# Optimization experiments

Measured on AMD Instinct MI355X. Metric: run time of the kernel, lower is better.

The kernel has to match this reference:

```python
import jax, jax.numpy as jnp
import numpy as np

N = 50000   # nodes
E = 800000  # directed edges (self-loops added inside reference)
F_IN, H, C = 128, 96, 32


def setup_inputs() -> dict:
    key = jax.random.key(0)
    ks = jax.random.split(key, 8)
    x = jax.random.normal(ks[0], (N, F_IN), dtype=jnp.float32)
    edge_index = jax.random.randint(ks[1], (2, E), 0, N, dtype=jnp.int64)
    W1 = jax.random.normal(ks[2], (F_IN, H), dtype=jnp.float32) * 0.05
    b1 = jnp.zeros((H,), dtype=jnp.float32)
    W2 = jax.random.normal(ks[3], (H, H), dtype=jnp.float32) * 0.05
    b2 = jnp.zeros((H,), dtype=jnp.float32)
    W3 = jax.random.normal(ks[4], (H, C), dtype=jnp.float32) * 0.05
    b3 = jnp.zeros((C,), dtype=jnp.float32)
    return {"x": x, "edge_index": edge_index, "W1": W1, "b1": b1,
            "W2": W2, "b2": b2, "W3": W3, "b3": b3}


def gcn_conv(x, W, b, src, dst, n):
    """PyG GCNConv: x' = D^{-1/2} (A+I) D^{-1/2} (x W) + b (self-loops in src/dst)."""
    xw = x @ W                                        # [n, out]
    ones = jnp.ones(src.shape[0], dtype=xw.dtype)
    deg = jax.ops.segment_sum(ones, dst, num_segments=n)
    dinv = jnp.where(deg > 0, jax.lax.rsqrt(jnp.maximum(deg, 1.0)), 0.0)
    norm = dinv[src] * dinv[dst]                      # [E+n]
    msg = norm[:, None] * xw[src]                     # gather + scale
    out = jax.ops.segment_sum(msg, dst, num_segments=n)  # scatter-add
    return out + b


def reference(x, edge_index, W1, b1, W2, b2, W3, b3):
    loop = jnp.arange(N, dtype=edge_index.dtype)
    src = jnp.concatenate([edge_index[0], loop])      # add self-loops once
    dst = jnp.concatenate([edge_index[1], loop])
    h = jax.nn.relu(gcn_conv(x, W1, b1, src, dst, N))   # dropout is identity (eval)
    h = jax.nn.relu(gcn_conv(h, W2, b2, src, dst, N))
    h = gcn_conv(h, W3, b3, src, dst, N)
    return jax.nn.log_softmax(h, axis=1)
```

## Files before the change

### kernel.cpp

```cpp
#include <hip/hip_runtime.h>
#include <hip/hip_fp16.h>


typedef _Float16 half8 __attribute__((ext_vector_type(8)));
typedef float f32x4 __attribute__((ext_vector_type(4)));

constexpr int CAP = 64;
constexpr int NPB = 128;
constexpr int NBINS_P = 512;
constexpr int EPB = 4096;
constexpr int BCAP = 2560;

__device__ inline unsigned char f_to_fp8(float f) {
    f = fminf(fmaxf(f, -448.0f), 448.0f);
    unsigned short u = __half_as_ushort(__float2half(f * 0.00390625f));
    unsigned short mag = (unsigned short)((u & 0x7FFF) + 0x40);
    return (unsigned char)(((u >> 8) & 0x80) | (mag >> 7));
}

__device__ inline float2 fp8x2_to_f2_scaled(unsigned int w) {
    unsigned int lo = ((w << 7) & 0x3F80u) | ((w << 8) & 0x8000u);
    unsigned int hi = ((w >> 1) & 0x3F80u) | (w & 0x8000u);
    union { unsigned int u; __half2 h; } cv;
    cv.u = lo | (hi << 16);
    return __half22float2(cv.h);
}

__device__ inline float4 fp8x4_to_f4_scaled(unsigned int w) {
    float2 lo = fp8x2_to_f2_scaled(w & 0xFFFFu);
    float2 hi = fp8x2_to_f2_scaled(w >> 16);
    return {lo.x, lo.y, hi.x, hi.y};
}

__global__ __launch_bounds__(256) void prep_kernel(const int* __restrict__ ei, int twoE,
                                                   int* __restrict__ flags,
                                                   int* __restrict__ bin_cnt,
                                                   const float* __restrict__ W1,
                                                   const float* __restrict__ W2,
                                                   const float* __restrict__ W3,
                                                   __half* __restrict__ Wt1,
                                                   __half* __restrict__ Wt2,
                                                   __half* __restrict__ Wt3) {
    if (blockIdx.x == 0) {
        if (threadIdx.x < 8) flags[threadIdx.x] = 0;
        for (int b = threadIdx.x; b < NBINS_P; b += 256) bin_cnt[b] = 0;
        __syncthreads();
        int c = 0;
        for (int j = threadIdx.x; j < 2048 && j < twoE; j += 256) {
            if ((j & 1) && ei[j] != 0) c++;
        }
        if (c) atomicAdd(&flags[4], c);
        return;
    }
    int i = (blockIdx.x - 1) * 256 + threadIdx.x;
    if (i < 128 * 96) {
        int f = i / 128, k = i - f * 128;
        Wt1[i] = __float2half(W1[(size_t)k * 96 + f]);
    } else if (i < 128 * 96 + 96 * 96) {
        int j = i - 128 * 96;
        int f = j / 96, k = j - f * 96;
        Wt2[j] = __float2half(W2[(size_t)k * 96 + f]);
    } else if (i < 128 * 96 + 96 * 96 + 96 * 32) {
        int j = i - 128 * 96 - 96 * 96;
        int f = j / 96, k = j - f * 96;
        Wt3[j] = __float2half(W3[(size_t)k * 32 + f]);
    }
}

__device__ inline int ld_idx(const int* ei, int half_, int i, int E, bool i64) {
    return i64 ? ei[2 * (half_ * (size_t)E + i)] : ei[half_ * (size_t)E + i];
}

__global__ __launch_bounds__(256) void part_kernel(const int* __restrict__ ei,
                                                   const int* __restrict__ flags,
                                                   int* __restrict__ bin_cnt,
                                                   int* __restrict__ bins, int E, int n) {
    __shared__ int hist[NBINS_P], excl[NBINS_P], cur[NBINS_P], gpos[NBINS_P];
    __shared__ int tmp[256];
    __shared__ int stage[EPB];
    const int tid = threadIdx.x;
    const bool i64 = (flags[4] == 0);
    for (int b = tid; b < NBINS_P; b += 256) hist[b] = 0;
    __syncthreads();

    int v[EPB / 256];
    const int base = blockIdx.x * EPB;
#pragma unroll
    for (int j = 0; j < EPB / 256; j++) {
        int i = base + j * 256 + tid;
        v[j] = -1;
        if (i < E) {
            int s = ld_idx(ei, 0, i, E, i64);
            int d = ld_idx(ei, 1, i, E, i64);
            if ((unsigned)s < (unsigned)n && (unsigned)d < (unsigned)n) {
                int bin = d >> 7, ln = d & 127;
                v[j] = (bin << 23) | (ln << 16) | s;
                atomicAdd(&hist[bin], 1);
            }
        }
    }
    __syncthreads();
    int a0 = hist[2 * tid], a1 = hist[2 * tid + 1];
    int pairsum = a0 + a1;
    tmp[tid] = pairsum;
    __syncthreads();
    for (int off = 1; off < 256; off <<= 1) {
        int t = (tid >= off) ? tmp[tid - off] : 0;
        __syncthreads();
        tmp[tid] += t;
        __syncthreads();
    }
    int S = tmp[tid] - pairsum;
    excl[2 * tid] = S;
    excl[2 * tid + 1] = S + a0;
    cur[2 * tid] = S;
    cur[2 * tid + 1] = S + a0;
    __syncthreads();
    for (int b = tid; b < NBINS_P; b += 256)
        gpos[b] = hist[b] ? atomicAdd(&bin_cnt[b], hist[b]) : 0;
#pragma unroll
    for (int j = 0; j < EPB / 256; j++) {
        if (v[j] != -1) {
            int bin = ((unsigned)v[j]) >> 23;
            int p = atomicAdd(&cur[bin], 1);
            stage[p] = v[j];
        }
    }
    __syncthreads();
    int total = excl[NBINS_P - 1] + hist[NBINS_P - 1];
    for (int i = tid; i < total; i += 256) {
        int w = stage[i];
        int bin = ((unsigned)w) >> 23;
        int k = gpos[bin] + (i - excl[bin]);
        if (k < BCAP) bins[(size_t)bin * BCAP + k] = w;
    }
}

__global__ __launch_bounds__(256) void build_kernel(const int* __restrict__ bin_cnt,
                                                    const int* __restrict__ bins,
                                                    int* __restrict__ cnt,
                                                    unsigned short* __restrict__ csr, int n) {
    __shared__ unsigned short lcsr[NPB * CAP];
    __shared__ int lcnt[NPB];
    const int b = blockIdx.x, tid = threadIdx.x;
    for (int i = tid; i < NPB; i += 256) lcnt[i] = 0;
    __syncthreads();
    int m = min(bin_cnt[b], BCAP);
    for (int i = tid; i < m; i += 256) {
        int w = bins[(size_t)b * BCAP + i];
        int ln = (w >> 16) & 127;
        int p = atomicAdd(&lcnt[ln], 1);
        if (p < CAP) lcsr[ln * CAP + p] = (unsigned short)(w & 0xFFFF);
    }
    __syncthreads();
    const int node0 = b * NPB;
    const unsigned int* l32 = (const unsigned int*)lcsr;
    unsigned int* c32 = (unsigned int*)(csr + (size_t)node0 * CAP);
    for (int i = tid; i < NPB * CAP / 2; i += 256) {
        int node = node0 + (i >> 5);
        if (node < n) c32[i] = l32[i];
    }
    for (int t = tid; t < NPB; t += 256)
        if (node0 + t < n) cnt[node0 + t] = lcnt[t];
}

__device__ inline half8 to_h8(float4 u0, float4 u1) {
    half8 r;
    r[0] = (_Float16)u0.x; r[1] = (_Float16)u0.y; r[2] = (_Float16)u0.z; r[3] = (_Float16)u0.w;
    r[4] = (_Float16)u1.x; r[5] = (_Float16)u1.y; r[6] = (_Float16)u1.z; r[7] = (_Float16)u1.w;
    return r;
}

template <int K, int F, bool XF32, bool OUT8>
__global__ __launch_bounds__(256) void gemm_mfma(const void* __restrict__ X,
                                                 const __half* __restrict__ Wt,
                                                 const int* __restrict__ cnt,
                                                 void* __restrict__ out, int n) {
    constexpr int KP = K + 8;
    constexpr int FT = F / 16;
    constexpr int KC = K / 32;
    __shared__ _Float16 Wl[F * KP];
    for (int i = threadIdx.x; i < F * (K / 8); i += 256) {
        int f = i / (K / 8), c = i - f * (K / 8);
        *(half8*)&Wl[f * KP + c * 8] = *(const half8*)&Wt[(size_t)f * K + c * 8];
    }
    __syncthreads();
    const int wave = threadIdx.x >> 6, lane = threadIdx.x & 63;
    const int node0 = (blockIdx.x * 4 + wave) * 16;
    if (node0 >= n) return;
    const int m = lane & 15, q = lane >> 4;
    const int arow = min(node0 + m, n - 1);

    half8 af[KC];
    if (XF32) {
        const float* xp = (const float*)X + (size_t)arow * K + q * 8;
#pragma unroll
        for (int kc = 0; kc < KC; kc++) {
            float4 u0 = *(const float4*)(xp + kc * 32);
            float4 u1 = *(const float4*)(xp + kc * 32 + 4);
            af[kc] = to_h8(u0, u1);
        }
    } else {
        const __half* xp = (const __half*)X + (size_t)arow * K + q * 8;
#pragma unroll
        for (int kc = 0; kc < KC; kc++) af[kc] = *(const half8*)(xp + kc * 32);
    }

    f32x4 acc[FT];
#pragma unroll
    for (int t = 0; t < FT; t++) acc[t] = (f32x4)0.f;
#pragma unroll
    for (int kc = 0; kc < KC; kc++) {
#pragma unroll
        for (int t = 0; t < FT; t++) {
            half8 b = *(const half8*)&Wl[(t * 16 + m) * KP + kc * 32 + q * 8];
            acc[t] = __builtin_amdgcn_mfma_f32_16x16x32_f16(af[kc], b, acc[t], 0, 0, 0);
        }
    }
    float dv[4];
#pragma unroll
    for (int r = 0; r < 4; r++) {
        int node = node0 + q * 4 + r;
        dv[r] = (node < n) ? rsqrtf(1.0f + (float)cnt[node]) : 0.f;
    }
#pragma unroll
    for (int t = 0; t < FT; t++)
#pragma unroll
        for (int r = 0; r < 4; r++) {
            int node = node0 + q * 4 + r;
            if (node < n) {
                float vv = acc[t][r] * dv[r];
                if (OUT8)
                    ((unsigned char*)out)[(size_t)node * F + t * 16 + m] = f_to_fp8(vv);
                else
                    ((__half*)out)[(size_t)node * F + t * 16 + m] = __float2half(vv);
            }
        }
}

__global__ __launch_bounds__(256) void agg96_fp8(const unsigned char* __restrict__ xws,
                                                 const int* __restrict__ cnt,
                                                 const unsigned short* __restrict__ csr,
                                                 const float* __restrict__ bias,
                                                 __half* __restrict__ out, int n) {
    int node = blockIdx.x * 4 + (threadIdx.x >> 6);
    int lane = threadIdx.x & 63;
    if (node >= n) return;
    const int g = lane < 24 ? 0 : 1;
    const int c = g ? lane - 24 : lane;
    const bool act = lane < 48;
    int deg = cnt[node];
    int m = min(deg, CAP);
    float dvs = rsqrtf(1.0f + (float)deg) * 256.0f;
    const uint4* r4 = (const uint4*)(csr + (size_t)node * CAP);
    float4 a = {0.f, 0.f, 0.f, 0.f};
    if (lane < 24) {
        unsigned int w = *(const unsigned int*)(xws + (size_t)node * 96 + c * 4);
        a = fp8x4_to_f4_scaled(w);
    }
    int e = 0;
#define G96_U(pr_) (g ? ((pr_) >> 16) : ((pr_) & 0xFFFF))
#define G96_LD(u_) (*(const unsigned int*)(xws + (size_t)(u_) * 96 + c * 4))
    for (; e + 16 <= m; e += 16) {
        uint4 pa = r4[e >> 3], pb = r4[(e >> 3) + 1];
        if (act) {
            unsigned int w0 = G96_LD(G96_U(pa.x)), w1 = G96_LD(G96_U(pa.y));
            unsigned int w2 = G96_LD(G96_U(pa.z)), w3 = G96_LD(G96_U(pa.w));
            unsigned int w4 = G96_LD(G96_U(pb.x)), w5 = G96_LD(G96_U(pb.y));
            unsigned int w6 = G96_LD(G96_U(pb.z)), w7 = G96_LD(G96_U(pb.w));
            float4 f;
            f = fp8x4_to_f4_scaled(w0); a.x += f.x; a.y += f.y; a.z += f.z; a.w += f.w;
            f = fp8x4_to_f4_scaled(w1); a.x += f.x; a.y += f.y; a.z += f.z; a.w += f.w;
            f = fp8x4_to_f4_scaled(w2); a.x += f.x; a.y += f.y; a.z += f.z; a.w += f.w;
            f = fp8x4_to_f4_scaled(w3); a.x += f.x; a.y += f.y; a.z += f.z; a.w += f.w;
            f = fp8x4_to_f4_scaled(w4); a.x += f.x; a.y += f.y; a.z += f.z; a.w += f.w;
            f = fp8x4_to_f4_scaled(w5); a.x += f.x; a.y += f.y; a.z += f.z; a.w += f.w;
            f = fp8x4_to_f4_scaled(w6); a.x += f.x; a.y += f.y; a.z += f.z; a.w += f.w;
            f = fp8x4_to_f4_scaled(w7); a.x += f.x; a.y += f.y; a.z += f.z; a.w += f.w;
        }
    }
    if (e + 8 <= m) {
        uint4 pa = r4[e >> 3];
        if (act) {
            unsigned int w0 = G96_LD(G96_U(pa.x)), w1 = G96_LD(G96_U(pa.y));
            unsigned int w2 = G96_LD(G96_U(pa.z)), w3 = G96_LD(G96_U(pa.w));
            float4 f;
            f = fp8x4_to_f4_scaled(w0); a.x += f.x; a.y += f.y; a.z += f.z; a.w += f.w;
            f = fp8x4_to_f4_scaled(w1); a.x += f.x; a.y += f.y; a.z += f.z; a.w += f.w;
            f = fp8x4_to_f4_scaled(w2); a.x += f.x; a.y += f.y; a.z += f.z; a.w += f.w;
            f = fp8x4_to_f4_scaled(w3); a.x += f.x; a.y += f.y; a.z += f.z; a.w += f.w;
        }
        e += 8;
    }
    if (e + 4 <= m) {
        const unsigned int* r2 = (const unsigned int*)r4;
        unsigned int p0 = r2[e >> 1], p1 = r2[(e >> 1) + 1];
        if (act) {
            unsigned int w0 = G96_LD(G96_U(p0)), w1 = G96_LD(G96_U(p1));
            float4 f;
            f = fp8x4_to_f4_scaled(w0); a.x += f.x; a.y += f.y; a.z += f.z; a.w += f.w;
            f = fp8x4_to_f4_scaled(w1); a.x += f.x; a.y += f.y; a.z += f.z; a.w += f.w;
        }
        e += 4;
    }
    if (e + 2 <= m) {
        unsigned int p0 = ((const unsigned int*)r4)[e >> 1];
        if (act) {
            unsigned int w0 = G96_LD(G96_U(p0));
            float4 f = fp8x4_to_f4_scaled(w0);
            a.x += f.x; a.y += f.y; a.z += f.z; a.w += f.w;
        }
        e += 2;
    }
    if (e < m && lane < 24) {
        int u = ((const unsigned short*)r4)[e];
        float4 f = fp8x4_to_f4_scaled(G96_LD(u));
        a.x += f.x; a.y += f.y; a.z += f.z; a.w += f.w;
    }
#undef G96_U
#undef G96_LD
    float px = __shfl(a.x, lane + 24);
    float py = __shfl(a.y, lane + 24);
    float pz = __shfl(a.z, lane + 24);
    float pw = __shfl(a.w, lane + 24);
    if (lane < 24) {
        a.x += px; a.y += py; a.z += pz; a.w += pw;
        float4 bb = *(const float4*)&bias[c * 4];
        float r0 = fmaxf(fmaf(dvs, a.x, bb.x), 0.f);
        float r1 = fmaxf(fmaf(dvs, a.y, bb.y), 0.f);
        float r2 = fmaxf(fmaf(dvs, a.z, bb.z), 0.f);
        float r3 = fmaxf(fmaf(dvs, a.w, bb.w), 0.f);
        union { __half2 h[2]; uint2 u; } pk;
        pk.h[0] = __floats2half2_rn(r0, r1);
        pk.h[1] = __floats2half2_rn(r2, r3);
        *(uint2*)(out + (size_t)node * 96 + c * 4) = pk.u;
    }
}

__global__ __launch_bounds__(256) void agg32_lsm(const __half* __restrict__ xws,
                                                 const int* __restrict__ cnt,
                                                 const unsigned short* __restrict__ csr,
                                                 const float* __restrict__ bias,
                                                 float* __restrict__ out, int n) {
    int node = blockIdx.x * 4 + (threadIdx.x >> 6);
    int lane = threadIdx.x & 63;
    if (node >= n) return;
    const int g = lane >> 4, l = lane & 15;
    int deg = cnt[node];
    int m = min(deg, CAP);
    float dv = rsqrtf(1.0f + (float)deg);
    const uint4* r4 = (const uint4*)(csr + (size_t)node * CAP);
    float2 a = {0.f, 0.f};
    if (g == 0) a = __half22float2(*(const __half2*)(xws + (size_t)node * 32 + l * 2));
    auto ext = [](uint4 p, int j) -> int {
        unsigned int h = (j & 4) ? ((j & 2) ? p.w : p.z) : ((j & 2) ? p.y : p.x);
        return (j & 1) ? (int)(h >> 16) : (int)(h & 0xFFFF);
    };
    int e = 0;
    for (; e + 16 <= m; e += 16) {
        uint4 pa = r4[e >> 3], pb = r4[(e >> 3) + 1];
        int u0 = ext(pa, g), u1 = ext(pa, g + 4);
        int u2 = ext(pb, g), u3 = ext(pb, g + 4);
        float2 f0 = __half22float2(*(const __half2*)(xws + (size_t)u0 * 32 + l * 2));
        float2 f1 = __half22float2(*(const __half2*)(xws + (size_t)u1 * 32 + l * 2));
        float2 f2 = __half22float2(*(const __half2*)(xws + (size_t)u2 * 32 + l * 2));
        float2 f3 = __half22float2(*(const __half2*)(xws + (size_t)u3 * 32 + l * 2));
        a.x += f0.x + f1.x + f2.x + f3.x;
        a.y += f0.y + f1.y + f2.y + f3.y;
    }
    if (e + 8 <= m) {
        uint4 pa = r4[e >> 3];
        int u0 = ext(pa, g), u1 = ext(pa, g + 4);
        float2 f0 = __half22float2(*(const __half2*)(xws + (size_t)u0 * 32 + l * 2));
        float2 f1 = __half22float2(*(const __half2*)(xws + (size_t)u1 * 32 + l * 2));
        a.x += f0.x + f1.x;
        a.y += f0.y + f1.y;
        e += 8;
    }
    if (e + 4 <= m) {
        unsigned int p0 = ((const unsigned int*)r4)[e >> 1];
        unsigned int p1 = ((const unsigned int*)r4)[(e >> 1) + 1];
        unsigned int h = (g & 2) ? p1 : p0;
        int u = (g & 1) ? (int)(h >> 16) : (int)(h & 0xFFFF);
        float2 f = __half22float2(*(const __half2*)(xws + (size_t)u * 32 + l * 2));
        a.x += f.x; a.y += f.y;
        e += 4;
    }
    for (; e < m; e++) {
        if (g == 0) {
            int u = ((const unsigned short*)r4)[e];
            float2 f = __half22float2(*(const __half2*)(xws + (size_t)u * 32 + l * 2));
            a.x += f.x; a.y += f.y;
        }
    }
    a.x += __shfl_xor(a.x, 16); a.y += __shfl_xor(a.y, 16);
    a.x += __shfl_xor(a.x, 32); a.y += __shfl_xor(a.y, 32);
    if (g == 0) {
        float2 b = *(const float2*)&bias[l * 2];
        float rx = fmaf(dv, a.x, b.x), ry = fmaf(dv, a.y, b.y);
        float mx = fmaxf(rx, ry);
        mx = fmaxf(mx, __shfl_xor(mx, 1));
        mx = fmaxf(mx, __shfl_xor(mx, 2));
        mx = fmaxf(mx, __shfl_xor(mx, 4));
        mx = fmaxf(mx, __shfl_xor(mx, 8));
        float s = expf(rx - mx) + expf(ry - mx);
        s += __shfl_xor(s, 1);
        s += __shfl_xor(s, 2);
        s += __shfl_xor(s, 4);
        s += __shfl_xor(s, 8);
        float ls = logf(s);
        ((float2*)out)[(size_t)node * 16 + l] = {rx - mx - ls, ry - mx - ls};
    }
}

extern "C" void kernel_launch(void* const* d_in, const int* in_sizes, int n_in,
                              void* d_out, int out_size, void* d_ws, size_t ws_size,
                              hipStream_t stream) {
    const float* x  = (const float*)d_in[0];
    const int*   ei = (const int*)d_in[1];
    const float* W1 = (const float*)d_in[2];
    const float* b1 = (const float*)d_in[3];
    const float* W2 = (const float*)d_in[4];
    const float* b2 = (const float*)d_in[5];
    const float* W3 = (const float*)d_in[6];
    const float* b3 = (const float*)d_in[7];
    float* out = (float*)d_out;

    const int N_ = in_sizes[0] / 128;
    const int E_ = in_sizes[1] / 2;
    const int NBINS = (N_ + NPB - 1) / NPB;

    char* base = (char*)d_ws;
    size_t off = 0;
    auto take = [&](size_t bytes) {
        void* p = base + off;
        off = (off + bytes + 255) & ~(size_t)255;
        return p;
    };
    int*    flags   = (int*)take(4 * 8);
    int*    bin_cnt = (int*)take(4 * NBINS_P);
    int*    bins    = (int*)take(4 * (size_t)NBINS * BCAP);
    int*    cnt     = (int*)take(4 * (size_t)N_);
    unsigned short* csr = (unsigned short*)take(2 * (size_t)N_ * CAP);
    __half* Wt1     = (__half*)take(2 * 128 * 96);
    __half* Wt2     = (__half*)take(2 * 96 * 96);
    __half* Wt3     = (__half*)take(2 * 96 * 32);
    unsigned char* bufA = (unsigned char*)take(2 * (size_t)N_ * 96);
    __half* bufB    = (__half*)take(2 * (size_t)N_ * 96);

    const int prepBlocks = 1 + (128 * 96 + 96 * 96 + 96 * 32 + 255) / 256;
    prep_kernel<<<prepBlocks, 256, 0, stream>>>(ei, in_sizes[1], flags, bin_cnt,
                                                W1, W2, W3, Wt1, Wt2, Wt3);
    part_kernel<<<(E_ + EPB - 1) / EPB, 256, 0, stream>>>(ei, flags, bin_cnt, bins, E_, N_);
    build_kernel<<<NBINS, 256, 0, stream>>>(bin_cnt, bins, cnt, csr, N_);

    const int gGemm = (N_ + 63) / 64;
    const int gAgg  = (N_ + 3) / 4;

    gemm_mfma<128, 96, true, true><<<gGemm, 256, 0, stream>>>(x, Wt1, cnt, bufA, N_);
    agg96_fp8<<<gAgg, 256, 0, stream>>>(bufA, cnt, csr, b1, bufB, N_);
    gemm_mfma<96, 96, false, true><<<gGemm, 256, 0, stream>>>(bufB, Wt2, cnt, bufA, N_);
    agg96_fp8<<<gAgg, 256, 0, stream>>>(bufA, cnt, csr, b2, bufB, N_);
    gemm_mfma<96, 32, false, false><<<gGemm, 256, 0, stream>>>(bufB, Wt3, cnt, bufA, N_);
    agg32_lsm<<<gAgg, 256, 0, stream>>>((const __half*)bufA, cnt, csr, b3, out, N_);
}
```

Before: 225.2 us.

## Split fp8 hidden features into two half-planes and aggregate each separately

The GEMM now writes its fp8 output as two planes of 48 features, each padded to a 64-byte row, and the 96-wide aggregation is replaced by a 48-wide kernel launched over twice as many blocks, one half per plane. Each wave uses four groups of 16 lanes, 12 of them active, so every group gathers a different neighbor and the partial sums are combined with xor shuffles. The aim is to make each gathered row a single 64-byte-aligned segment with better cache-line use, and to raise parallelism across the gather. In exchange, the CSR index lists are read twice and a quarter of the lanes sit idle.

```diff
diff --git a/kernel.cpp b/kernel.cpp
--- a/kernel.cpp
+++ b/kernel.cpp
@@ -30,6 +30,11 @@
     float2 lo = fp8x2_to_f2_scaled(w & 0xFFFFu);
     float2 hi = fp8x2_to_f2_scaled(w >> 16);
     return {lo.x, lo.y, hi.x, hi.y};
+}
+
+__device__ inline int ext8(uint4 p, int j) {
+    unsigned int h = (j & 4) ? ((j & 2) ? p.w : p.z) : ((j & 2) ? p.y : p.x);
+    return (j & 1) ? (int)(h >> 16) : (int)(h & 0xFFFFu);
 }
 
 __global__ __launch_bounds__(256) void prep_kernel(const int* __restrict__ ei, int twoE,
@@ -230,110 +235,101 @@
             int node = node0 + q * 4 + r;
             if (node < n) {
                 float vv = acc[t][r] * dv[r];
-                if (OUT8)
-                    ((unsigned char*)out)[(size_t)node * F + t * 16 + m] = f_to_fp8(vv);
-                else
+                if (OUT8) {
+                    constexpr int h = (OUT8 && 0) ? 0 : 0;
+                    int f = t * 16 + m;
+                    int hh = (f >= 48) ? 1 : 0;
+                    ((unsigned char*)out)[(size_t)hh * ((size_t)n * 64) +
+                                          (size_t)node * 64 + (f - hh * 48)] = f_to_fp8(vv);
+                    (void)h;
+                } else {
                     ((__half*)out)[(size_t)node * F + t * 16 + m] = __float2half(vv);
+                }
             }
         }
 }
 
-__global__ __launch_bounds__(256) void agg96_fp8(const unsigned char* __restrict__ xws,
+__global__ __launch_bounds__(256) void agg48_fp8(const unsigned char* __restrict__ xws,
                                                  const int* __restrict__ cnt,
                                                  const unsigned short* __restrict__ csr,
                                                  const float* __restrict__ bias,
-                                                 __half* __restrict__ out, int n) {
-    int node = blockIdx.x * 4 + (threadIdx.x >> 6);
-    int lane = threadIdx.x & 63;
+                                                 __half* __restrict__ out, int n, int gHalf) {
+    const int b = blockIdx.x;
+    const int half = (b >= gHalf) ? 1 : 0;
+    const int node = (b - half * gHalf) * 4 + (threadIdx.x >> 6);
     if (node >= n) return;
-    const int g = lane < 24 ? 0 : 1;
-    const int c = g ? lane - 24 : lane;
-    const bool act = lane < 48;
-    int deg = cnt[node];
-    int m = min(deg, CAP);
-    float dvs = rsqrtf(1.0f + (float)deg) * 256.0f;
+    const int lane = threadIdx.x & 63;
+    const int g = lane >> 4, l = lane & 15;
+    const bool act = l < 12;
+    const int deg = cnt[node];
+    const int m = min(deg, CAP);
+    const float dvs = rsqrtf(1.0f + (float)deg) * 256.0f;
+    const unsigned char* __restrict__ pl = xws + (size_t)half * ((size_t)n * 64);
     const uint4* r4 = (const uint4*)(csr + (size_t)node * CAP);
+    const unsigned int* r2 = (const unsigned int*)r4;
     float4 a = {0.f, 0.f, 0.f, 0.f};
-    if (lane < 24) {
-        unsigned int w = *(const unsigned int*)(xws + (size_t)node * 96 + c * 4);
-        a = fp8x4_to_f4_scaled(w);
-    }
+    if (g == 0 && act)
+        a = fp8x4_to_f4_scaled(*(const unsigned int*)(pl + (size_t)node * 64 + l * 4));
+#define A48_LD(u_) (*(const unsigned int*)(pl + (size_t)(u_) * 64 + l * 4))
+#define A48_ACC(w_) { float4 f_ = fp8x4_to_f4_scaled(w_); \
+                      a.x += f_.x; a.y += f_.y; a.z += f_.z; a.w += f_.w; }
     int e = 0;
-#define G96_U(pr_) (g ? ((pr_) >> 16) : ((pr_) & 0xFFFF))
-#define G96_LD(u_) (*(const unsigned int*)(xws + (size_t)(u_) * 96 + c * 4))
     for (; e + 16 <= m; e += 16) {
         uint4 pa = r4[e >> 3], pb = r4[(e >> 3) + 1];
         if (act) {
-            unsigned int w0 = G96_LD(G96_U(pa.x)), w1 = G96_LD(G96_U(pa.y));
-            unsigned int w2 = G96_LD(G96_U(pa.z)), w3 = G96_LD(G96_U(pa.w));
-            unsigned int w4 = G96_LD(G96_U(pb.x)), w5 = G96_LD(G96_U(pb.y));
-            unsigned int w6 = G96_LD(G96_U(pb.z)), w7 = G96_LD(G96_U(pb.w));
-            float4 f;
-            f = fp8x4_to_f4_scaled(w0); a.x += f.x; a.y += f.y; a.z += f.z; a.w += f.w;
-            f = fp8x4_to_f4_scaled(w1); a.x += f.x; a.y += f.y; a.z += f.z; a.w += f.w;
-            f = fp8x4_to_f4_scaled(w2); a.x += f.x; a.y += f.y; a.z += f.z; a.w += f.w;
-            f = fp8x4_to_f4_scaled(w3); a.x += f.x; a.y += f.y; a.z += f.z; a.w += f.w;
-            f = fp8x4_to_f4_scaled(w4); a.x += f.x; a.y += f.y; a.z += f.z; a.w += f.w;
-            f = fp8x4_to_f4_scaled(w5); a.x += f.x; a.y += f.y; a.z += f.z; a.w += f.w;
-            f = fp8x4_to_f4_scaled(w6); a.x += f.x; a.y += f.y; a.z += f.z; a.w += f.w;
-            f = fp8x4_to_f4_scaled(w7); a.x += f.x; a.y += f.y; a.z += f.z; a.w += f.w;
+            unsigned int w0 = A48_LD(ext8(pa, g));
+            unsigned int w1 = A48_LD(ext8(pa, g + 4));
+            unsigned int w2 = A48_LD(ext8(pb, g));
+            unsigned int w3 = A48_LD(ext8(pb, g + 4));
+            A48_ACC(w0) A48_ACC(w1) A48_ACC(w2) A48_ACC(w3)
         }
     }
     if (e + 8 <= m) {
         uint4 pa = r4[e >> 3];
         if (act) {
-            unsigned int w0 = G96_LD(G96_U(pa.x)), w1 = G96_LD(G96_U(pa.y));
-            unsigned int w2 = G96_LD(G96_U(pa.z)), w3 = G96_LD(G96_U(pa.w));
-            float4 f;
-            f = fp8x4_to_f4_scaled(w0); a.x += f.x; a.y += f.y; a.z += f.z; a.w += f.w;
-            f = fp8x4_to_f4_scaled(w1); a.x += f.x; a.y += f.y; a.z += f.z; a.w += f.w;
-            f = fp8x4_to_f4_scaled(w2); a.x += f.x; a.y += f.y; a.z += f.z; a.w += f.w;
-            f = fp8x4_to_f4_scaled(w3); a.x += f.x; a.y += f.y; a.z += f.z; a.w += f.w;
+            unsigned int w0 = A48_LD(ext8(pa, g));
+            unsigned int w1 = A48_LD(ext8(pa, g + 4));
+            A48_ACC(w0) A48_ACC(w1)
         }
         e += 8;
     }
     if (e + 4 <= m) {
-        const unsigned int* r2 = (const unsigned int*)r4;
         unsigned int p0 = r2[e >> 1], p1 = r2[(e >> 1) + 1];
         if (act) {
-            unsigned int w0 = G96_LD(G96_U(p0)), w1 = G96_LD(G96_U(p1));
-            float4 f;
-            f = fp8x4_to_f4_scaled(w0); a.x += f.x; a.y += f.y; a.z += f.z; a.w += f.w;
-            f = fp8x4_to_f4_scaled(w1); a.x += f.x; a.y += f.y; a.z += f.z; a.w += f.w;
+            unsigned int h = (g & 2) ? p1 : p0;
+            int u = (g & 1) ? (int)(h >> 16) : (int)(h & 0xFFFFu);
+            A48_ACC(A48_LD(u))
         }
         e += 4;
     }
     if (e + 2 <= m) {
-        unsigned int p0 = ((const unsigned int*)r4)[e >> 1];
-        if (act) {
-            unsigned int w0 = G96_LD(G96_U(p0));
-            float4 f = fp8x4_to_f4_scaled(w0);
-            a.x += f.x; a.y += f.y; a.z += f.z; a.w += f.w;
+        unsigned int p0 = r2[e >> 1];
+        if (g < 2 && act) {
+            int u = g ? (int)(p0 >> 16) : (int)(p0 & 0xFFFFu);
+            A48_ACC(A48_LD(u))
         }
         e += 2;
     }
-    if (e < m && lane < 24) {
+    if (e < m && g == 0 && act) {
         int u = ((const unsigned short*)r4)[e];
-        float4 f = fp8x4_to_f4_scaled(G96_LD(u));
-        a.x += f.x; a.y += f.y; a.z += f.z; a.w += f.w;
-    }
-#undef G96_U
-#undef G96_LD
-    float px = __shfl(a.x, lane + 24);
-    float py = __shfl(a.y, lane + 24);
-    float pz = __shfl(a.z, lane + 24);
-    float pw = __shfl(a.w, lane + 24);
-    if (lane < 24) {
-        a.x += px; a.y += py; a.z += pz; a.w += pw;
-        float4 bb = *(const float4*)&bias[c * 4];
+        A48_ACC(A48_LD(u))
+    }
+#undef A48_LD
+#undef A48_ACC
+    a.x += __shfl_xor(a.x, 16); a.y += __shfl_xor(a.y, 16);
+    a.z += __shfl_xor(a.z, 16); a.w += __shfl_xor(a.w, 16);
+    a.x += __shfl_xor(a.x, 32); a.y += __shfl_xor(a.y, 32);
+    a.z += __shfl_xor(a.z, 32); a.w += __shfl_xor(a.w, 32);
+    if (g == 0 && act) {
+        float4 bb = *(const float4*)&bias[half * 48 + l * 4];
         float r0 = fmaxf(fmaf(dvs, a.x, bb.x), 0.f);
         float r1 = fmaxf(fmaf(dvs, a.y, bb.y), 0.f);
-        float r2 = fmaxf(fmaf(dvs, a.z, bb.z), 0.f);
+        float r2v = fmaxf(fmaf(dvs, a.z, bb.z), 0.f);
         float r3 = fmaxf(fmaf(dvs, a.w, bb.w), 0.f);
         union { __half2 h[2]; uint2 u; } pk;
         pk.h[0] = __floats2half2_rn(r0, r1);
-        pk.h[1] = __floats2half2_rn(r2, r3);
-        *(uint2*)(out + (size_t)node * 96 + c * 4) = pk.u;
+        pk.h[1] = __floats2half2_rn(r2v, r3);
+        *(uint2*)(out + (size_t)node * 96 + half * 48 + l * 4) = pk.u;
     }
 }
 
@@ -352,15 +348,11 @@
     const uint4* r4 = (const uint4*)(csr + (size_t)node * CAP);
     float2 a = {0.f, 0.f};
     if (g == 0) a = __half22float2(*(const __half2*)(xws + (size_t)node * 32 + l * 2));
-    auto ext = [](uint4 p, int j) -> int {
-        unsigned int h = (j & 4) ? ((j & 2) ? p.w : p.z) : ((j & 2) ? p.y : p.x);
-        return (j & 1) ? (int)(h >> 16) : (int)(h & 0xFFFF);
-    };
     int e = 0;
     for (; e + 16 <= m; e += 16) {
         uint4 pa = r4[e >> 3], pb = r4[(e >> 3) + 1];
-        int u0 = ext(pa, g), u1 = ext(pa, g + 4);
-        int u2 = ext(pb, g), u3 = ext(pb, g + 4);
+        int u0 = ext8(pa, g), u1 = ext8(pa, g + 4);
+        int u2 = ext8(pb, g), u3 = ext8(pb, g + 4);
         float2 f0 = __half22float2(*(const __half2*)(xws + (size_t)u0 * 32 + l * 2));
         float2 f1 = __half22float2(*(const __half2*)(xws + (size_t)u1 * 32 + l * 2));
         float2 f2 = __half22float2(*(const __half2*)(xws + (size_t)u2 * 32 + l * 2));
@@ -370,7 +362,7 @@
     }
     if (e + 8 <= m) {
         uint4 pa = r4[e >> 3];
-        int u0 = ext(pa, g), u1 = ext(pa, g + 4);
+        int u0 = ext8(pa, g), u1 = ext8(pa, g + 4);
         float2 f0 = __half22float2(*(const __half2*)(xws + (size_t)u0 * 32 + l * 2));
         float2 f1 = __half22float2(*(const __half2*)(xws + (size_t)u1 * 32 + l * 2));
         a.x += f0.x + f1.x;
@@ -458,9 +450,9 @@
     const int gAgg  = (N_ + 3) / 4;
 
     gemm_mfma<128, 96, true, true><<<gGemm, 256, 0, stream>>>(x, Wt1, cnt, bufA, N_);
-    agg96_fp8<<<gAgg, 256, 0, stream>>>(bufA, cnt, csr, b1, bufB, N_);
+    agg48_fp8<<<2 * gAgg, 256, 0, stream>>>(bufA, cnt, csr, b1, bufB, N_, gAgg);
     gemm_mfma<96, 96, false, true><<<gGemm, 256, 0, stream>>>(bufB, Wt2, cnt, bufA, N_);
-    agg96_fp8<<<gAgg, 256, 0, stream>>>(bufA, cnt, csr, b2, bufB, N_);
+    agg48_fp8<<<2 * gAgg, 256, 0, stream>>>(bufA, cnt, csr, b2, bufB, N_, gAgg);
     gemm_mfma<96, 32, false, false><<<gGemm, 256, 0, stream>>>(bufB, Wt3, cnt, bufA, N_);
     agg32_lsm<<<gAgg, 256, 0, stream>>>((const __half*)bufA, cnt, csr, b3, out, N_);
 }
```

Result: slower. 258.7 us (+14.8%).
